# Kernel tuning notes

Hardware: AMD Instinct MI355X
Metric: run time of the kernel (lower is better)

## Reference

```python
import jax, jax.numpy as jnp
import numpy as np
from jax import lax

B, S, V, E, H, NH = 32, 512, 30000, 300, 200, 4
ENC = 2 * H           # bidirectional encoder size = 400
DH = ENC // NH        # head dim = 100
BUDGET = 20.0         # percent of length kept by sparseMAP
SCALING = 1.0 / 0.001 # eval-mode temperature (module sets 0.001 at test time)
NEG = -1e9


def setup_inputs():
    key = jax.random.key(0)
    ks = jax.random.split(key, 16)
    lengths = jax.random.randint(ks[0], (B,), S // 2, S + 1)
    mask = jnp.arange(S)[None, :] < lengths[:, None]          # prefix mask [B,S]
    x = jax.random.randint(ks[1], (B, S), 0, V)
    p = lambda k, sh: jax.random.normal(k, sh, jnp.float32) * 0.05
    return {
        "x": x, "mask": mask,
        "embed_table": p(ks[2], (V, E)),
        "w_ih_f": p(ks[3], (4 * H, E)), "w_hh_f": p(ks[4], (4 * H, H)), "b_f": jnp.zeros((4 * H,), jnp.float32),
        "w_ih_b": p(ks[5], (4 * H, E)), "w_hh_b": p(ks[6], (4 * H, H)), "b_b": jnp.zeros((4 * H,), jnp.float32),
        "q_state": p(ks[7], (ENC,)),
        "W_q": p(ks[8], (ENC, ENC)), "W_k": p(ks[9], (ENC, ENC)), "W_v": p(ks[10], (ENC, ENC)),
        "W_out": p(ks[11], (ENC, ENC)),
        "W_head": p(ks[12], (ENC, 1)), "b_head": jnp.zeros((1,), jnp.float32),
    }


def _lstm(xW, mask, W_hh):
    """Masked (packed-equivalent) LSTM. xW: [B,S,4H] precomputed input proj, mask [B,S] bool."""
    Bb, Ss, H4 = xW.shape
    Hh = H4 // 4
    def step(carry, t_in):
        h, c = carry
        g, m = t_in                             # g [B,4H], m [B,1] bool
        gates = g + h @ W_hh.T
        i, f, gg, o = jnp.split(gates, 4, axis=-1)
        c_new = jax.nn.sigmoid(f) * c + jax.nn.sigmoid(i) * jnp.tanh(gg)
        h_new = jax.nn.sigmoid(o) * jnp.tanh(c_new)
        return (jnp.where(m, h_new, h), jnp.where(m, c_new, c)), jnp.where(m, h_new, 0.0)
    init = (jnp.zeros((Bb, Hh), xW.dtype), jnp.zeros((Bb, Hh), xW.dtype))
    xs = (jnp.swapaxes(xW, 0, 1), jnp.swapaxes(mask[..., None], 0, 1))
    _, outs = lax.scan(step, init, xs)
    return jnp.swapaxes(outs, 0, 1)


def _proj_capped_simplex(theta, k):
    """SparseMAP budget QP: argmin ||mu - theta||^2 s.t. 0<=mu<=1, sum(mu)=k.
    Bisection on threshold tau (non-diff), then exact differentiable tau on the free set."""
    th = lax.stop_gradient(theta)
    lo = jnp.min(th) - 1.0
    hi = jnp.max(th)
    def body(_, ab):
        lo, hi = ab
        mid = 0.5 * (lo + hi)
        too_big = jnp.sum(jnp.clip(th - mid, 0.0, 1.0)) > k
        return (jnp.where(too_big, mid, lo), jnp.where(too_big, hi, mid))
    lo, hi = lax.fori_loop(0, 60, body, (lo, hi))
    tau0 = 0.5 * (lo + hi)
    mu0 = th - tau0
    free = (mu0 > 0.0) & (mu0 < 1.0)
    nU = jnp.sum(mu0 >= 1.0).astype(theta.dtype)
    nS = jnp.sum(free).astype(theta.dtype)
    tau = (jnp.sum(jnp.where(free, theta, 0.0)) + nU - k) / jnp.maximum(nS, 1.0)
    tau = jnp.where(nS > 0, tau, tau0)
    return jnp.clip(theta - tau, 0.0, 1.0)


def _forward(x, mask, embed_table, w_ih_f, w_hh_f, b_f, w_ih_b, w_hh_b, b_b,
             q_state, W_q, W_k, W_v, W_out, W_head, b_head):
    lengths = mask.sum(1)                                   # [B] int
    emb = embed_table[x]                                    # [B,S,E] (dropout off: eval)
    # forward direction
    h_f = _lstm(emb @ w_ih_f.T + b_f, mask, w_hh_f)         # [B,S,H]
    # backward direction: reverse each sample within its length (packed semantics)
    t = jnp.arange(S)
    idx = jnp.clip(lengths[:, None] - 1 - t[None, :], 0, S - 1)   # [B,S], involution on valid part
    emb_rev = jnp.take_along_axis(emb, idx[..., None], axis=1)
    h_b_rev = _lstm(emb_rev @ w_ih_b.T + b_b, mask, w_hh_b)
    h_b = jnp.take_along_axis(h_b_rev, idx[..., None], axis=1)
    h_b = jnp.where(mask[..., None], h_b, 0.0)
    h = jnp.concatenate([h_f, h_b], axis=-1)                # [B,S,ENC]
    # Hopfield pooling with learned query state, per-sample sparseMAP top-k budget
    q = (q_state @ W_q).reshape(NH, DH)                     # learned pooling query
    K = (h @ W_k).reshape(B, S, NH, DH)
    Vv = (h @ W_v).reshape(B, S, NH, DH)
    scores = SCALING * jnp.einsum('hd,bshd->bhs', q, K)     # [B,NH,S]
    scores = jnp.where(mask[:, None, :], scores, NEG)
    kbud = jnp.round(BUDGET / 100.0 * lengths.astype(jnp.float32))   # per-sample budget
    proj = jax.vmap(jax.vmap(_proj_capped_simplex, (0, None)), (0, 0))
    p = proj(scores, kbud)                                  # [B,NH,S] sparse marginals
    pooled = jnp.einsum('bhs,bshd->bhd', p, Vv).reshape(B, ENC) @ W_out
    y = jax.nn.sigmoid(pooled @ W_head + b_head)            # [B,1]
    z = jnp.where(mask, p.mean(1), 0.0)                     # [B,S] rationale
    return y, z


def reference(x, mask, embed_table, w_ih_f, w_hh_f, b_f, w_ih_b, w_hh_b, b_b,
              q_state, W_q, W_k, W_v, W_out, W_head, b_head):
    return _forward(x, mask, embed_table, w_ih_f, w_hh_f, b_f, w_ih_b, w_hh_b, b_b,
                    q_state, W_q, W_k, W_v, W_out, W_head, b_head)
```

## Files before the change

### kernel.cpp

```cpp
#include <hip/hip_runtime.h>
#include <hip/hip_bf16.h>
#include <math.h>

#define B_   32
#define S_   512
#define V_   30000
#define E_   300
#define H_   200
#define NH_  4
#define ENC_ 400
#define G4_  800
#define NEGV  (-1e9f)
#define SCALE_ 1000.0f

typedef _Float16 half2v __attribute__((ext_vector_type(2)));
typedef _Float16 f16x8  __attribute__((ext_vector_type(8)));
typedef float    f32x4  __attribute__((ext_vector_type(4)));

#if defined(__has_builtin)
#if __has_builtin(__builtin_amdgcn_fdot2)
#define FDOT2(a,b,c) __builtin_amdgcn_fdot2((a),(b),(c),false)
#endif
#endif
#ifndef FDOT2
#define FDOT2(a,b,c) fmaf((float)(a)[1],(float)(b)[1], fmaf((float)(a)[0],(float)(b)[0],(c)))
#endif

#define OF_QVEC  320000ull
#define OF_WKQ   320448ull
#define OF_THETA 322048ull
#define OF_MU    387584ull
#define OF_HP    453120ull
#define OF_LEN   504320ull
#define OF_XWF   504384ull
#define OF_XWB   13611584ull
#define OF_HF    26718784ull
#define OF_HB    29995584ull

__global__ void k_lengths(const void* __restrict__ mask, int* __restrict__ lengths) {
  int b = blockIdx.x, lane = threadIdx.x;
  const unsigned char* mb = (const unsigned char*)mask;
  int mode;
  if (mb[1] != 0) mode = 0;
  else if (((const int*)mask)[1] != 0) mode = 1;
  else mode = 2;
  int cnt = 0;
  for (int s = lane; s < S_; s += 64) {
    int v;
    if (mode == 0)      v = mb[b*S_ + s] ? 1 : 0;
    else if (mode == 1) v = ((const int*)mask)[b*S_ + s] ? 1 : 0;
    else                v = ((const long long*)mask)[b*S_ + s] ? 1 : 0;
    cnt += v;
  }
  for (int off = 32; off; off >>= 1) cnt += __shfl_xor(cnt, off);
  if (lane == 0) lengths[b] = cnt;
}

__global__ void k_qvec(const float* __restrict__ qs, const float* __restrict__ Wq,
                       float* __restrict__ qvec) {
  __shared__ float qsl[ENC_];
  int t = threadIdx.x;
  if (t < ENC_) qsl[t] = qs[t];
  __syncthreads();
  if (t < ENC_) {
    float acc = 0.f;
    for (int i = 0; i < ENC_; ++i) acc += qsl[i] * Wq[(size_t)i*ENC_ + t];
    qvec[t] = acc;
  }
}

__global__ void k_wkq(const float* __restrict__ Wk, const float* __restrict__ qvec,
                      float* __restrict__ wkq) {
  int t = threadIdx.x;
  int e = blockIdx.x*64 + (t >> 2);
  int head = t & 3;
  if (e < ENC_) {
    float acc = 0.f;
    const float* row = Wk + (size_t)e*ENC_ + head*100;
    const float* qv  = qvec + head*100;
    for (int d = 0; d < 100; ++d) acc += row[d]*qv[d];
    wkq[e*4 + head] = acc;
  }
}

__global__ __launch_bounds__(256) void k_gemm_mfma(
    const int* __restrict__ x, const float* __restrict__ emb,
    const float* __restrict__ wf, const float* __restrict__ wb,
    const float* __restrict__ bf, const float* __restrict__ bb,
    float* __restrict__ xWf, float* __restrict__ xWb)
{
  __shared__ int xid[128];
  __shared__ __align__(16) _Float16 sA[128][40];
  __shared__ __align__(16) _Float16 sB[64][40];
  const int t = threadIdx.x;
  const int row0 = blockIdx.x * 128;
  const int col0 = blockIdx.y * 64;
  if (t < 128) xid[t] = x[row0 + t];
  const int w = t >> 6, lane = t & 63;
  const int wr = w >> 1, wc = w & 1;
  f32x4 acc[4][2] = {};
  const int ar = t >> 1, ah = t & 1;
  const int bc = t >> 2, bq = t & 3;
  const int colg = col0 + bc;
  const float* wsrc = (colg < 800) ? (wf + (size_t)colg*300)
                                   : (wb + (size_t)(colg-800)*300);
  __syncthreads();
  const float* asrc = emb + (size_t)xid[ar]*300;
  for (int kc = 0; kc < 10; ++kc) {
    const int k0 = kc*32;
    {
      const int kb = k0 + ah*16;
      _Float16 tmp[16];
      if (kb + 15 < 300) {
        #pragma unroll
        for (int q = 0; q < 4; ++q) {
          float4 a = *(const float4*)(asrc + kb + 4*q);
          tmp[4*q]  =(_Float16)a.x; tmp[4*q+1]=(_Float16)a.y;
          tmp[4*q+2]=(_Float16)a.z; tmp[4*q+3]=(_Float16)a.w;
        }
      } else {
        #pragma unroll
        for (int i = 0; i < 16; ++i)
          tmp[i] = (_Float16)((kb+i < 300) ? asrc[kb+i] : 0.f);
      }
      *(f16x8*)&sA[ar][ah*16]   = *(f16x8*)&tmp[0];
      *(f16x8*)&sA[ar][ah*16+8] = *(f16x8*)&tmp[8];
    }
    {
      const int kb = k0 + bq*8;
      _Float16 tmp[8];
      if (kb + 7 < 300) {
        #pragma unroll
        for (int q = 0; q < 2; ++q) {
          float4 a = *(const float4*)(wsrc + kb + 4*q);
          tmp[4*q]  =(_Float16)a.x; tmp[4*q+1]=(_Float16)a.y;
          tmp[4*q+2]=(_Float16)a.z; tmp[4*q+3]=(_Float16)a.w;
        }
      } else {
        #pragma unroll
        for (int i = 0; i < 8; ++i)
          tmp[i] = (_Float16)((kb+i < 300) ? wsrc[kb+i] : 0.f);
      }
      *(f16x8*)&sB[bc][bq*8] = *(f16x8*)&tmp[0];
    }
    __syncthreads();
    const int fr = lane & 15, kg = lane >> 4;
    f16x8 b0 = *(const f16x8*)&sB[wc*32 + fr][kg*8];
    f16x8 b1 = *(const f16x8*)&sB[wc*32 + 16 + fr][kg*8];
    #pragma unroll
    for (int m = 0; m < 4; ++m) {
      f16x8 afrag = *(const f16x8*)&sA[wr*64 + m*16 + fr][kg*8];
      acc[m][0] = __builtin_amdgcn_mfma_f32_16x16x32_f16(afrag, b0, acc[m][0], 0,0,0);
      acc[m][1] = __builtin_amdgcn_mfma_f32_16x16x32_f16(afrag, b1, acc[m][1], 0,0,0);
    }
    __syncthreads();
  }
  const int crb = (lane >> 4) * 4, ccol = lane & 15;
  #pragma unroll
  for (int n = 0; n < 2; ++n) {
    int colg2 = col0 + wc*32 + n*16 + ccol;
    bool isF = colg2 < 800;
    int colo = isF ? colg2 : colg2 - 800;
    float bias = isF ? bf[colo] : bb[colo];
    float* dst = isF ? xWf : xWb;
    #pragma unroll
    for (int m = 0; m < 4; ++m) {
      int row = row0 + wr*64 + m*16 + crb;
      #pragma unroll
      for (int r = 0; r < 4; ++r)
        dst[(size_t)(row+r)*800 + colo] = acc[m][n][r] + bias;
    }
  }
}

__global__ __launch_bounds__(1024, 1) void k_lstm_v2(
    const float* __restrict__ xWf, const float* __restrict__ xWb,
    const float* __restrict__ whhf, const float* __restrict__ whhb,
    const int* __restrict__ lengths,
    float* __restrict__ h_f, float* __restrict__ h_b)
{
  const int bid = blockIdx.x;
  const int dir = bid >> 5, b = bid & 31;
  const float* __restrict__ xW  = dir ? xWb : xWf;
  const float* __restrict__ whh = dir ? whhb : whhf;
  float* __restrict__ hout      = dir ? h_b : h_f;
  const int len = lengths[b];
  const int t = threadIdx.x;
  const int active = (t < G4_);

  __shared__ __align__(16) _Float16 hbh[200];
  __shared__ float gact[G4_];

  half2v w[100];
  if (active) {
    const float* rp = whh + (size_t)t*H_;
    #pragma unroll
    for (int j = 0; j < 50; ++j) {
      float2 a = *(const float2*)(rp + 2*j);
      w[j] = half2v{(_Float16)a.x, (_Float16)a.y};
    }
    #pragma unroll
    for (int j = 0; j < 50; ++j) {
      float2 a = *(const float2*)(rp + 100 + 2*j);
      w[50+j] = half2v{(_Float16)a.x, (_Float16)a.y};
    }
  }
  if (t < 200) hbh[t] = (_Float16)0.f;
  float cst = 0.f;
  const float* xbase = xW + (size_t)b*S_*G4_;
  const int isTanh = (t >= 400) && (t < 600);
  __syncthreads();

  for (int step = 0; step < len; ++step) {
    const int pos = dir ? (len-1-step) : step;
    if (active) {
      float xv = xbase[(size_t)pos*G4_ + t];
      float a0 = 0.f, a1 = 0.f;
      #pragma unroll
      for (int j = 0; j < 12; ++j) {
        float4 h4 = *(const float4*)&hbh[8*j];
        a0 = FDOT2(w[4*j],   __builtin_bit_cast(half2v, h4.x), a0);
        a1 = FDOT2(w[4*j+1], __builtin_bit_cast(half2v, h4.y), a1);
        a0 = FDOT2(w[4*j+2], __builtin_bit_cast(half2v, h4.z), a0);
        a1 = FDOT2(w[4*j+3], __builtin_bit_cast(half2v, h4.w), a1);
      }
      {
        float2 h2 = *(const float2*)&hbh[96];
        a0 = FDOT2(w[48], __builtin_bit_cast(half2v, h2.x), a0);
        a1 = FDOT2(w[49], __builtin_bit_cast(half2v, h2.y), a1);
      }
      #pragma unroll
      for (int j = 0; j < 12; ++j) {
        float4 h4 = *(const float4*)&hbh[100 + 8*j];
        a0 = FDOT2(w[50+4*j],   __builtin_bit_cast(half2v, h4.x), a0);
        a1 = FDOT2(w[50+4*j+1], __builtin_bit_cast(half2v, h4.y), a1);
        a0 = FDOT2(w[50+4*j+2], __builtin_bit_cast(half2v, h4.z), a0);
        a1 = FDOT2(w[50+4*j+3], __builtin_bit_cast(half2v, h4.w), a1);
      }
      {
        float2 h2 = *(const float2*)&hbh[196];
        a0 = FDOT2(w[98], __builtin_bit_cast(half2v, h2.x), a0);
        a1 = FDOT2(w[99], __builtin_bit_cast(half2v, h2.y), a1);
      }
      float pre = a0 + a1 + xv;
      float act;
      if (isTanh) {
        float gc = fminf(fmaxf(pre, -10.f), 10.f);
        float e2 = __expf(2.f*gc);
        act = (e2-1.f)/(e2+1.f);
      } else {
        act = 1.f/(1.f+__expf(-pre));
      }
      gact[t] = act;
    }
    __syncthreads();
    if (t < 200) {
      float ig = gact[t], fg = gact[200+t], gg = gact[400+t], og = gact[600+t];
      cst = fg*cst + ig*gg;
      float cc = fminf(fmaxf(cst, -10.f), 10.f);
      float ec = __expf(2.f*cc);
      float hn = og*((ec-1.f)/(ec+1.f));
      hout[((size_t)b*S_ + pos)*H_ + t] = hn;
      hbh[t] = (_Float16)hn;
    }
    __syncthreads();
  }
}

__global__ __launch_bounds__(256) void k_scores(
    const float* __restrict__ hf, const float* __restrict__ hb,
    const float* __restrict__ wkq, const int* __restrict__ lengths,
    float* __restrict__ theta)
{
  int wid = blockIdx.x*4 + (threadIdx.x >> 6);
  int lane = threadIdx.x & 63;
  int b = wid >> 9, s = wid & 511;
  const float* hfr = hf + ((size_t)b*S_ + s)*H_;
  const float* hbr = hb + ((size_t)b*S_ + s)*H_;
  bool valid = s < lengths[b];
  float a0=0.f, a1=0.f, a2=0.f, a3=0.f;
  if (valid) {
    for (int e = lane; e < ENC_; e += 64) {
      float hv = (e < H_) ? hfr[e] : hbr[e-H_];
      float4 w = *(const float4*)(wkq + e*4);
      a0 += hv*w.x; a1 += hv*w.y; a2 += hv*w.z; a3 += hv*w.w;
    }
    for (int off = 32; off; off >>= 1) {
      a0 += __shfl_xor(a0, off); a1 += __shfl_xor(a1, off);
      a2 += __shfl_xor(a2, off); a3 += __shfl_xor(a3, off);
    }
  }
  if (lane == 0) {
    size_t base = (size_t)b*2048 + s;
    theta[base       ] = valid ? SCALE_*a0 : NEGV;
    theta[base +  512] = valid ? SCALE_*a1 : NEGV;
    theta[base + 1024] = valid ? SCALE_*a2 : NEGV;
    theta[base + 1536] = valid ? SCALE_*a3 : NEGV;
  }
}

__global__ void k_sparsemap(const float* __restrict__ theta, const int* __restrict__ lengths,
                            float* __restrict__ mu) {
  int pid = blockIdx.x;
  int lane = threadIdx.x;
  const float* th = theta + (size_t)pid*512;
  float v[8];
  #pragma unroll
  for (int i = 0; i < 8; ++i) v[i] = th[i*64 + lane];
  float kf = rintf(0.2f * (float)lengths[pid >> 2]);
  float mn = v[0], mx = v[0];
  #pragma unroll
  for (int i = 1; i < 8; ++i) { mn = fminf(mn, v[i]); mx = fmaxf(mx, v[i]); }
  for (int off = 32; off; off >>= 1) {
    mn = fminf(mn, __shfl_xor(mn, off)); mx = fmaxf(mx, __shfl_xor(mx, off));
  }
  float lo = mn - 1.f, hi = mx;
  for (int it = 0; it < 60; ++it) {
    float mid = 0.5f*(lo + hi);
    float s = 0.f;
    #pragma unroll
    for (int i = 0; i < 8; ++i) s += fminf(fmaxf(v[i]-mid, 0.f), 1.f);
    for (int off = 32; off; off >>= 1) s += __shfl_xor(s, off);
    bool big = s > kf;
    lo = big ? mid : lo;
    hi = big ? hi : mid;
  }
  float tau0 = 0.5f*(lo + hi);
  float fs = 0.f, nU = 0.f, nS = 0.f;
  #pragma unroll
  for (int i = 0; i < 8; ++i) {
    float m0 = v[i] - tau0;
    if (m0 >= 1.f) nU += 1.f;
    else if (m0 > 0.f) { fs += v[i]; nS += 1.f; }
  }
  for (int off = 32; off; off >>= 1) {
    fs += __shfl_xor(fs, off); nU += __shfl_xor(nU, off); nS += __shfl_xor(nS, off);
  }
  float tau = (fs + nU - kf) / fmaxf(nS, 1.f);
  tau = (nS > 0.f) ? tau : tau0;
  float* mo = mu + (size_t)pid*512;
  #pragma unroll
  for (int i = 0; i < 8; ++i) mo[i*64 + lane] = fminf(fmaxf(v[i]-tau, 0.f), 1.f);
}

__global__ __launch_bounds__(512) void k_hp(
    const float* __restrict__ mu, const float* __restrict__ hf,
    const float* __restrict__ hb, float* __restrict__ hp)
{
  __shared__ float mul[512];
  int pid = blockIdx.x, b = pid >> 2;
  int t = threadIdx.x;
  mul[t] = mu[(size_t)pid*512 + t];
  __syncthreads();
  if (t < ENC_) {
    const float* hsrc = (t < H_) ? (hf + t) : (hb + (t - H_));
    float acc = 0.f;
    for (int s = 0; s < 512; ++s) {
      float m = mul[s];
      if (m != 0.f) acc += m * hsrc[((size_t)b*S_ + s)*H_];
    }
    hp[(size_t)pid*ENC_ + t] = acc;
  }
}

__global__ __launch_bounds__(512) void k_head(
    const float* __restrict__ hp, const float* __restrict__ Wv,
    const float* __restrict__ Wout, const float* __restrict__ Wh,
    const float* __restrict__ bh, float* __restrict__ out)
{
  __shared__ float hpl[1600];
  __shared__ float ppl[ENC_];
  __shared__ float ojl[ENC_];
  __shared__ float red[512];
  int b = blockIdx.x, t = threadIdx.x;
  for (int i = t; i < 1600; i += 512) hpl[i] = hp[(size_t)b*1600 + i];
  __syncthreads();
  if (t < ENC_) {
    int head = t / 100;
    float acc = 0.f;
    for (int e = 0; e < ENC_; ++e) acc += hpl[head*ENC_ + e] * Wv[(size_t)e*ENC_ + t];
    ppl[t] = acc;
  }
  __syncthreads();
  if (t < ENC_) {
    float acc = 0.f;
    for (int c = 0; c < ENC_; ++c) acc += ppl[c] * Wout[(size_t)c*ENC_ + t];
    ojl[t] = acc;
  }
  __syncthreads();
  red[t] = (t < ENC_) ? ojl[t]*Wh[t] : 0.f;
  __syncthreads();
  for (int sft = 256; sft; sft >>= 1) {
    if (t < sft) red[t] += red[t+sft];
    __syncthreads();
  }
  if (t == 0) out[b] = 1.f/(1.f + expf(-(red[0] + bh[0])));
}

__global__ void k_z(const float* __restrict__ mu, const int* __restrict__ lengths,
                    float* __restrict__ out) {
  int idx = blockIdx.x*256 + threadIdx.x;
  int b = idx >> 9, s = idx & 511;
  float zz = 0.f;
  if (s < lengths[b]) {
    size_t base = (size_t)b*2048 + s;
    zz = 0.25f*(mu[base] + mu[base+512] + mu[base+1024] + mu[base+1536]);
  }
  out[32 + idx] = zz;
}

extern "C" void kernel_launch(void* const* d_in, const int* in_sizes, int n_in,
                              void* d_out, int out_size, void* d_ws, size_t ws_size,
                              hipStream_t stream) {
  const int*   x    = (const int*)d_in[0];
  const void*  mask = d_in[1];
  const float* emb  = (const float*)d_in[2];
  const float* wihf = (const float*)d_in[3];
  const float* whhf = (const float*)d_in[4];
  const float* bf   = (const float*)d_in[5];
  const float* wihb = (const float*)d_in[6];
  const float* whhb = (const float*)d_in[7];
  const float* bb   = (const float*)d_in[8];
  const float* qs   = (const float*)d_in[9];
  const float* Wq   = (const float*)d_in[10];
  const float* Wk   = (const float*)d_in[11];
  const float* Wv   = (const float*)d_in[12];
  const float* Wout = (const float*)d_in[13];
  const float* Wh   = (const float*)d_in[14];
  const float* bh   = (const float*)d_in[15];
  float* out = (float*)d_out;
  float* W = (float*)d_ws;
  int* lengths = (int*)(W + OF_LEN);

  k_lengths<<<32, 64, 0, stream>>>(mask, lengths);
  k_qvec<<<1, 512, 0, stream>>>(qs, Wq, W+OF_QVEC);
  k_wkq<<<7, 256, 0, stream>>>(Wk, W+OF_QVEC, W+OF_WKQ);
  k_gemm_mfma<<<dim3(128, 25), 256, 0, stream>>>(x, emb, wihf, wihb, bf, bb,
                                                 W+OF_XWF, W+OF_XWB);
  k_lstm_v2<<<64, 1024, 0, stream>>>(W+OF_XWF, W+OF_XWB, whhf, whhb,
                                     lengths, W+OF_HF, W+OF_HB);
  k_scores<<<4096, 256, 0, stream>>>(W+OF_HF, W+OF_HB, W+OF_WKQ, lengths, W+OF_THETA);
  k_sparsemap<<<128, 64, 0, stream>>>(W+OF_THETA, lengths, W+OF_MU);
  k_hp<<<128, 512, 0, stream>>>(W+OF_MU, W+OF_HF, W+OF_HB, W+OF_HP);
  k_head<<<32, 512, 0, stream>>>(W+OF_HP, Wv, Wout, Wh, bh, out);
  k_z<<<64, 256, 0, stream>>>(W+OF_MU, lengths, out);
}
```

Baseline: 877.7 us.

## Restructure LSTM recurrence to one barrier per step with per-unit gate ownership

The LSTM kernel is reorganised so each group of 16 lanes owns one hidden unit and all four of its gates. Each lane holds a quarter slice of the four weight rows and combines partial dot products with cross-lane shuffles. The hidden state is double-buffered in shared memory, which removes the intermediate gate-activation buffer and one of the two block barriers per timestep. The block shrinks to 832 threads and every lane computes the activations redundantly, trading some extra ALU work and shuffles for shorter serial latency per step.

```diff
diff --git a/kernel.cpp b/kernel.cpp
--- a/kernel.cpp
+++ b/kernel.cpp
@@ -173,7 +173,9 @@
   }
 }
 
-__global__ __launch_bounds__(1024, 1) void k_lstm_v2(
+__global__
+__attribute__((amdgpu_flat_work_group_size(832, 832), amdgpu_waves_per_eu(1, 4)))
+void k_lstm_v3(
     const float* __restrict__ xWf, const float* __restrict__ xWb,
     const float* __restrict__ whhf, const float* __restrict__ whhb,
     const int* __restrict__ lengths,
@@ -186,82 +188,83 @@
   float* __restrict__ hout      = dir ? h_b : h_f;
   const int len = lengths[b];
   const int t = threadIdx.x;
-  const int active = (t < G4_);
-
-  __shared__ __align__(16) _Float16 hbh[200];
-  __shared__ float gact[G4_];
-
-  half2v w[100];
-  if (active) {
-    const float* rp = whh + (size_t)t*H_;
+  const int wave = t >> 6, lane = t & 63;
+  const int q = lane >> 4, u16 = lane & 15;
+  const int unit = wave*16 + u16;
+  const bool valid = (unit < H_);
+  const int uc = valid ? unit : (H_-1);
+
+  __shared__ __align__(16) _Float16 hxh[2][4][64];
+
+  half2v w0[25], w1[25], w2[25], w3[25];
+  {
+    const float* r0 = whh + ((size_t)(0*H_ + uc))*H_ + 50*q;
+    const float* r1 = whh + ((size_t)(1*H_ + uc))*H_ + 50*q;
+    const float* r2 = whh + ((size_t)(2*H_ + uc))*H_ + 50*q;
+    const float* r3 = whh + ((size_t)(3*H_ + uc))*H_ + 50*q;
     #pragma unroll
-    for (int j = 0; j < 50; ++j) {
-      float2 a = *(const float2*)(rp + 2*j);
-      w[j] = half2v{(_Float16)a.x, (_Float16)a.y};
-    }
-    #pragma unroll
-    for (int j = 0; j < 50; ++j) {
-      float2 a = *(const float2*)(rp + 100 + 2*j);
-      w[50+j] = half2v{(_Float16)a.x, (_Float16)a.y};
-    }
-  }
-  if (t < 200) hbh[t] = (_Float16)0.f;
+    for (int j = 0; j < 25; ++j) {
+      float2 a0 = *(const float2*)(r0 + 2*j);
+      float2 a1 = *(const float2*)(r1 + 2*j);
+      float2 a2 = *(const float2*)(r2 + 2*j);
+      float2 a3 = *(const float2*)(r3 + 2*j);
+      w0[j] = half2v{(_Float16)a0.x, (_Float16)a0.y};
+      w1[j] = half2v{(_Float16)a1.x, (_Float16)a1.y};
+      w2[j] = half2v{(_Float16)a2.x, (_Float16)a2.y};
+      w3[j] = half2v{(_Float16)a3.x, (_Float16)a3.y};
+    }
+  }
+
+  if (t < 128) ((unsigned int*)&hxh[0][0][0])[t] = 0u;
   float cst = 0.f;
   const float* xbase = xW + (size_t)b*S_*G4_;
-  const int isTanh = (t >= 400) && (t < 600);
   __syncthreads();
 
   for (int step = 0; step < len; ++step) {
     const int pos = dir ? (len-1-step) : step;
-    if (active) {
-      float xv = xbase[(size_t)pos*G4_ + t];
-      float a0 = 0.f, a1 = 0.f;
+    const int p = step & 1;
+    const float* xr = xbase + (size_t)pos*G4_ + uc;
+    float xi = xr[0], xf = xr[H_], xg = xr[2*H_], xo = xr[3*H_];
+    const unsigned int* hq = (const unsigned int*)&hxh[p][q][0];
+    float a0 = 0.f, a1 = 0.f, a2 = 0.f, a3 = 0.f;
+    #pragma unroll
+    for (int jj = 0; jj < 6; ++jj) {
+      uint4 hw4 = *(const uint4*)&hq[4*jj];
       #pragma unroll
-      for (int j = 0; j < 12; ++j) {
-        float4 h4 = *(const float4*)&hbh[8*j];
-        a0 = FDOT2(w[4*j],   __builtin_bit_cast(half2v, h4.x), a0);
-        a1 = FDOT2(w[4*j+1], __builtin_bit_cast(half2v, h4.y), a1);
-        a0 = FDOT2(w[4*j+2], __builtin_bit_cast(half2v, h4.z), a0);
-        a1 = FDOT2(w[4*j+3], __builtin_bit_cast(half2v, h4.w), a1);
+      for (int e = 0; e < 4; ++e) {
+        unsigned int wv = (e==0)?hw4.x:(e==1)?hw4.y:(e==2)?hw4.z:hw4.w;
+        half2v hh = __builtin_bit_cast(half2v, wv);
+        const int j = 4*jj + e;
+        a0 = FDOT2(w0[j], hh, a0);
+        a1 = FDOT2(w1[j], hh, a1);
+        a2 = FDOT2(w2[j], hh, a2);
+        a3 = FDOT2(w3[j], hh, a3);
       }
-      {
-        float2 h2 = *(const float2*)&hbh[96];
-        a0 = FDOT2(w[48], __builtin_bit_cast(half2v, h2.x), a0);
-        a1 = FDOT2(w[49], __builtin_bit_cast(half2v, h2.y), a1);
-      }
-      #pragma unroll
-      for (int j = 0; j < 12; ++j) {
-        float4 h4 = *(const float4*)&hbh[100 + 8*j];
-        a0 = FDOT2(w[50+4*j],   __builtin_bit_cast(half2v, h4.x), a0);
-        a1 = FDOT2(w[50+4*j+1], __builtin_bit_cast(half2v, h4.y), a1);
-        a0 = FDOT2(w[50+4*j+2], __builtin_bit_cast(half2v, h4.z), a0);
-        a1 = FDOT2(w[50+4*j+3], __builtin_bit_cast(half2v, h4.w), a1);
-      }
-      {
-        float2 h2 = *(const float2*)&hbh[196];
-        a0 = FDOT2(w[98], __builtin_bit_cast(half2v, h2.x), a0);
-        a1 = FDOT2(w[99], __builtin_bit_cast(half2v, h2.y), a1);
-      }
-      float pre = a0 + a1 + xv;
-      float act;
-      if (isTanh) {
-        float gc = fminf(fmaxf(pre, -10.f), 10.f);
-        float e2 = __expf(2.f*gc);
-        act = (e2-1.f)/(e2+1.f);
-      } else {
-        act = 1.f/(1.f+__expf(-pre));
-      }
-      gact[t] = act;
-    }
-    __syncthreads();
-    if (t < 200) {
-      float ig = gact[t], fg = gact[200+t], gg = gact[400+t], og = gact[600+t];
-      cst = fg*cst + ig*gg;
-      float cc = fminf(fmaxf(cst, -10.f), 10.f);
-      float ec = __expf(2.f*cc);
-      float hn = og*((ec-1.f)/(ec+1.f));
-      hout[((size_t)b*S_ + pos)*H_ + t] = hn;
-      hbh[t] = (_Float16)hn;
+    }
+    {
+      half2v hh = __builtin_bit_cast(half2v, hq[24]);
+      a0 = FDOT2(w0[24], hh, a0);
+      a1 = FDOT2(w1[24], hh, a1);
+      a2 = FDOT2(w2[24], hh, a2);
+      a3 = FDOT2(w3[24], hh, a3);
+    }
+    a0 += __shfl_xor(a0, 16); a0 += __shfl_xor(a0, 32);
+    a1 += __shfl_xor(a1, 16); a1 += __shfl_xor(a1, 32);
+    a2 += __shfl_xor(a2, 16); a2 += __shfl_xor(a2, 32);
+    a3 += __shfl_xor(a3, 16); a3 += __shfl_xor(a3, 32);
+    float gi = a0 + xi, gf = a1 + xf, gg = a2 + xg, go = a3 + xo;
+    float ig = 1.f/(1.f+__expf(-gi));
+    float fg = 1.f/(1.f+__expf(-gf));
+    float og = 1.f/(1.f+__expf(-go));
+    float ggc = fminf(fmaxf(gg, -10.f), 10.f);
+    float eg = __expf(2.f*ggc);
+    cst = fg*cst + ig*((eg-1.f)/(eg+1.f));
+    float cc = fminf(fmaxf(cst, -10.f), 10.f);
+    float ec = __expf(2.f*cc);
+    float hn = og*((ec-1.f)/(ec+1.f));
+    if (valid && q == 0) {
+      hout[((size_t)b*S_ + pos)*H_ + unit] = hn;
+      hxh[p^1][unit/50][unit%50] = (_Float16)hn;
     }
     __syncthreads();
   }
@@ -437,8 +440,8 @@
   k_wkq<<<7, 256, 0, stream>>>(Wk, W+OF_QVEC, W+OF_WKQ);
   k_gemm_mfma<<<dim3(128, 25), 256, 0, stream>>>(x, emb, wihf, wihb, bf, bb,
                                                  W+OF_XWF, W+OF_XWB);
-  k_lstm_v2<<<64, 1024, 0, stream>>>(W+OF_XWF, W+OF_XWB, whhf, whhb,
-                                     lengths, W+OF_HF, W+OF_HB);
+  k_lstm_v3<<<64, 832, 0, stream>>>(W+OF_XWF, W+OF_XWB, whhf, whhb,
+                                    lengths, W+OF_HF, W+OF_HB);
   k_scores<<<4096, 256, 0, stream>>>(W+OF_HF, W+OF_HB, W+OF_WKQ, lengths, W+OF_THETA);
   k_sparsemap<<<128, 64, 0, stream>>>(W+OF_THETA, lengths, W+OF_MU);
   k_hp<<<128, 512, 0, stream>>>(W+OF_MU, W+OF_HF, W+OF_HB, W+OF_HP);
```

Result: slower. 1.122 ms (+27.9%).
